# Performance work log

Hardware: AMD Instinct MI355X
Metric: run time of the kernel (lower is better)

The kernel has to match this reference:

```python
import jax, jax.numpy as jnp
import numpy as np

LN_EPS = 1e-5
N_HEADS = 8

def _layernorm(x, g, b):
    mu = jnp.mean(x, axis=-1, keepdims=True)
    var = jnp.var(x, axis=-1, keepdims=True)
    return (x - mu) * jax.lax.rsqrt(var + LN_EPS) * g + b

def _posenc(seqlen, d_model, dtype):
    den = jnp.exp(-jnp.arange(0, d_model, 2, dtype=dtype) * (np.log(10000.0) / d_model))
    pos = jnp.arange(seqlen, dtype=dtype)[:, None]  # [S,1]
    pe = jnp.zeros((seqlen, d_model), dtype=dtype)
    pe = pe.at[:, 0::2].set(jnp.sin(pos * den))
    pe = pe.at[:, 1::2].set(jnp.cos(pos * den)[:, : d_model // 2])
    return pe  # [S,d]

def setup_inputs() -> dict:
    key = jax.random.key(0)
    ks = jax.random.split(key, 12)
    B, S, V, D, F, L, DL = 64, 256, 16, 512, 2048, 6, 256
    s = 0.05
    return {
        "src_pad": jax.random.normal(ks[0], (B, S, V), jnp.float32),
        "emb_w": jax.random.normal(ks[1], (D, V), jnp.float32) * s,
        "emb_b": jnp.zeros((D,), jnp.float32),
        "qkv_w": jax.random.normal(ks[2], (L, 3 * D, D), jnp.float32) * s,
        "qkv_b": jnp.zeros((L, 3 * D), jnp.float32),
        "out_w": jax.random.normal(ks[3], (L, D, D), jnp.float32) * s,
        "out_b": jnp.zeros((L, D), jnp.float32),
        "ff1_w": jax.random.normal(ks[4], (L, F, D), jnp.float32) * s,
        "ff1_b": jnp.zeros((L, F), jnp.float32),
        "ff2_w": jax.random.normal(ks[5], (L, D, F), jnp.float32) * s,
        "ff2_b": jnp.zeros((L, D), jnp.float32),
        "ln1_g": jnp.ones((L, D), jnp.float32),
        "ln1_b": jnp.zeros((L, D), jnp.float32),
        "ln2_g": jnp.ones((L, D), jnp.float32),
        "ln2_b": jnp.zeros((L, D), jnp.float32),
        "lat_w": jax.random.normal(ks[6], (DL, S * D), jnp.float32) * 0.005,
        "lat_b": jnp.zeros((DL,), jnp.float32),
        "head_w": jax.random.normal(ks[7], (1, DL), jnp.float32) * s,
        "head_b": jnp.zeros((1,), jnp.float32),
    }

def reference(src_pad, emb_w, emb_b, qkv_w, qkv_b, out_w, out_b,
              ff1_w, ff1_b, ff2_w, ff2_b, ln1_g, ln1_b, ln2_g, ln2_b,
              lat_w, lat_b, head_w, head_b):
    B, S, V = src_pad.shape
    D = emb_w.shape[0]
    L = qkv_w.shape[0]
    H = N_HEADS
    dh = D // H
    # batched replacement of the per-token Python-loop embedding
    x = jnp.einsum('bsv,dv->bsd', src_pad, emb_w) + emb_b
    x = x + _posenc(S, D, x.dtype)  # dropout is identity at eval
    scale = 1.0 / np.sqrt(dh)
    for l in range(L):  # post-norm PyTorch TransformerEncoderLayer, relu FFN
        qkv = jnp.einsum('bsd,ed->bse', x, qkv_w[l]) + qkv_b[l]  # [B,S,3D]
        q, k, v = jnp.split(qkv, 3, axis=-1)
        q = q.reshape(B, S, H, dh).transpose(0, 2, 1, 3)
        k = k.reshape(B, S, H, dh).transpose(0, 2, 1, 3)
        v = v.reshape(B, S, H, dh).transpose(0, 2, 1, 3)
        attn = jax.nn.softmax(jnp.einsum('bhqd,bhkd->bhqk', q, k) * scale, axis=-1)
        o = jnp.einsum('bhqk,bhkd->bhqd', attn, v).transpose(0, 2, 1, 3).reshape(B, S, D)
        o = jnp.einsum('bsd,ed->bse', o, out_w[l]) + out_b[l]
        x = _layernorm(x + o, ln1_g[l], ln1_b[l])
        h = jax.nn.relu(jnp.einsum('bsd,fd->bsf', x, ff1_w[l]) + ff1_b[l])
        h = jnp.einsum('bsf,df->bsd', h, ff2_w[l]) + ff2_b[l]
        x = _layernorm(x + h, ln2_g[l], ln2_b[l])
    mem = x.reshape(B, S * D) @ lat_w.T + lat_b  # [B, d_latent]
    pred = jax.nn.sigmoid(mem @ head_w.T + head_b)  # [B,1]
    return pred
```

## Files before the change

### kernel.cpp

```cpp
#include <hip/hip_runtime.h>
#include <hip/hip_bf16.h>
#include <cstdint>

#define DEV static __device__ __forceinline__

typedef __attribute__((ext_vector_type(8))) short bf16x8;
typedef __attribute__((ext_vector_type(4))) float f32x4;

DEV unsigned short f2bf(float f) {
  union { float f; unsigned u; } c; c.f = f;
  unsigned u = c.u;
  return (unsigned short)((u + 0x7fffu + ((u >> 16) & 1u)) >> 16);
}
DEV float bf2f(unsigned short h) {
  union { unsigned u; float f; } c; c.u = ((unsigned)h) << 16; return c.f;
}
DEV unsigned pack_bf16(float a, float b) {
  union { float f; unsigned u; } ca, cb; ca.f = a; cb.f = b;
  return __builtin_amdgcn_perm(cb.u + 0x8000u, ca.u + 0x8000u, 0x07060302u);
}

#define ASYNC_COPY16(gsrc, ldst)                                                      \
  __builtin_amdgcn_global_load_lds(                                                   \
      (const __attribute__((address_space(1))) void*)(unsigned long long)(gsrc),      \
      (__attribute__((address_space(3))) void*)(unsigned int)(unsigned long long)(ldst), \
      16, 0, 0)

__global__ void cvt4_kernel(const float* __restrict__ s, unsigned short* __restrict__ d) {
  size_t i = ((size_t)blockIdx.x * 256 + threadIdx.x) * 4;
  float4 v = *(const float4*)(s + i);
  d[i + 0] = f2bf(v.x);
  d[i + 1] = f2bf(v.y);
  d[i + 2] = f2bf(v.z);
  d[i + 3] = f2bf(v.w);
}

__global__ void embed_kernel(const float* __restrict__ src,
                             const float* __restrict__ emb_w,
                             const float* __restrict__ emb_b,
                             float* __restrict__ x,
                             unsigned short* __restrict__ xb) {
  const int bs = blockIdx.x;
  const int d = threadIdx.x;
  const int s = bs & 255;
  __shared__ float sv[16];
  if (d < 16) sv[d] = src[(size_t)bs * 16 + d];
  __syncthreads();
  const float* wr = emb_w + (size_t)d * 16;
  float acc = emb_b[d];
#pragma unroll
  for (int v = 0; v < 16; v++) acc += sv[v] * wr[v];
  const float den = __expf(-(float)(d & ~1) * (9.2103403719761836f / 512.f));
  const float arg = (float)s * den;
  acc += (d & 1) ? __cosf(arg) : __sinf(arg);
  x[(size_t)bs * 512 + d] = acc;
  xb[(size_t)bs * 512 + d] = f2bf(acc);
}

template <int BN, int MINW, int RELU, int OUT_BF16, int ADD_RES>
__global__ __launch_bounds__(256, MINW) void gemm_nt(
    const unsigned short* __restrict__ A,
    const unsigned short* __restrict__ B,
    const float* __restrict__ bias,
    const float* __restrict__ res,
    float* __restrict__ Cf,
    unsigned short* __restrict__ Cb,
    int M, int N, int K) {
  constexpr int MT = (BN == 128) ? 4 : 2;
  constexpr int NT = 4;
  __shared__ unsigned short As[128 * 64];
  __shared__ unsigned short Bs[BN * 64];
  const int tid = threadIdx.x;
  const int lane = tid & 63;
  const int w = tid >> 6;
  const int m0 = blockIdx.x * 128;
  const int n0 = blockIdx.y * BN;

  const int srow = lane >> 3;
  const int scol = (((lane & 7) ^ srow)) * 8;
  const unsigned short* gA0 = A + (size_t)(m0 + w * 32 + srow) * K + scol;
  unsigned short* lA0 = As + (w * 32) * 64;
  constexpr int BROWS = BN / 4 / 8;
  const unsigned short* gB0 = B + (size_t)(n0 + w * (BN / 4) + srow) * K + scol;
  unsigned short* lB0 = Bs + (w * (BN / 4)) * 64;

  const int wm = (BN == 128) ? (w >> 1) * 64 : w * 32;
  const int wn = (BN == 128) ? (w & 1) * 64 : 0;
  const int r16 = lane & 15;
  const int quad = lane >> 4;
  const int rsw = r16 & 7;

  f32x4 acc[MT][NT] = {};

  for (int k0 = 0; k0 < K; k0 += 64) {
#pragma unroll
    for (int i = 0; i < 4; i++)
      ASYNC_COPY16(gA0 + (size_t)(i * 8) * K + k0, lA0 + i * 512);
#pragma unroll
    for (int i = 0; i < BROWS; i++)
      ASYNC_COPY16(gB0 + (size_t)(i * 8) * K + k0, lB0 + i * 512);
    __syncthreads();
#pragma unroll
    for (int kh = 0; kh < 2; kh++) {
      const int ko = ((kh * 4 + quad) ^ rsw) * 8;
      bf16x8 xa[MT], wb[NT];
#pragma unroll
      for (int i = 0; i < MT; i++)
        xa[i] = *(const bf16x8*)(As + (wm + i * 16 + r16) * 64 + ko);
#pragma unroll
      for (int j = 0; j < NT; j++)
        wb[j] = *(const bf16x8*)(Bs + (wn + j * 16 + r16) * 64 + ko);
#pragma unroll
      for (int i = 0; i < MT; i++)
#pragma unroll
        for (int j = 0; j < NT; j++)
          acc[i][j] = __builtin_amdgcn_mfma_f32_16x16x32_bf16(wb[j], xa[i], acc[i][j], 0, 0, 0);
    }
    __syncthreads();
  }

  const int mb = m0 + wm + r16;
  const int nb = n0 + wn + quad * 4;
#pragma unroll
  for (int j = 0; j < NT; j++) {
    const int n = nb + j * 16;
    const float4 bv = *(const float4*)(bias + n);
#pragma unroll
    for (int i = 0; i < MT; i++) {
      const size_t off = (size_t)(mb + i * 16) * N + n;
      float4 v;
      v.x = acc[i][j][0] + bv.x;
      v.y = acc[i][j][1] + bv.y;
      v.z = acc[i][j][2] + bv.z;
      v.w = acc[i][j][3] + bv.w;
      if (ADD_RES) {
        const float4 rr = *(const float4*)(res + off);
        v.x += rr.x; v.y += rr.y; v.z += rr.z; v.w += rr.w;
      }
      if (RELU) {
        v.x = fmaxf(v.x, 0.f); v.y = fmaxf(v.y, 0.f);
        v.z = fmaxf(v.z, 0.f); v.w = fmaxf(v.w, 0.f);
      }
      if (OUT_BF16) {
        uint2 u;
        u.x = pack_bf16(v.x, v.y);
        u.y = pack_bf16(v.z, v.w);
        *(uint2*)(Cb + off) = u;
      } else {
        *(float4*)(Cf + off) = v;
      }
    }
  }
}

__global__ __launch_bounds__(256, 2) void attn_fused(
    const unsigned short* __restrict__ qkv,
    unsigned short* __restrict__ O) {
  __shared__ unsigned short Vt[64 * 264];
  __shared__ unsigned short Pl[32 * 264];
  __shared__ float redM[4][32];
  __shared__ float redS[4][32];
  const int tid = threadIdx.x;
  const int lane = tid & 63;
  const int w = tid >> 6;
  const int r16 = lane & 15;
  const int quad = lane >> 4;
  const int h = blockIdx.x & 7;
  const int b = blockIdx.x >> 3;

  {
    const int kp = w * 32 + (lane & 31);
    const int dhalf = lane >> 5;
    const unsigned short* vbase =
        qkv + (size_t)(b * 256 + 2 * kp) * 1536 + 1024 + h * 64;
    unsigned* dst = (unsigned*)Vt;
#pragma unroll
    for (int t = 0; t < 4; t++) {
      const int dc = dhalf + 2 * t;
      const uint4 a = *(const uint4*)(vbase + dc * 8);
      const uint4 bb = *(const uint4*)(vbase + 1536 + dc * 8);
      const unsigned* ap = (const unsigned*)&a;
      const unsigned* bp = (const unsigned*)&bb;
#pragma unroll
      for (int i = 0; i < 4; i++) {
        const unsigned lo = ap[i], hi = bp[i];
        dst[(dc * 8 + 2 * i) * 132 + kp] = (lo & 0xffffu) | (hi << 16);
        dst[(dc * 8 + 2 * i + 1) * 132 + kp] = (lo >> 16) | (hi & 0xffff0000u);
      }
    }
  }
  __syncthreads();

  const unsigned short* krow =
      qkv + (size_t)(b * 256 + r16) * 1536 + 512 + h * 64 + quad * 8;
  const unsigned short* qrow =
      qkv + (size_t)(b * 256 + r16) * 1536 + h * 64 + quad * 8;

  for (int qt = 0; qt < 8; qt++) {
    const int q0 = qt * 32;
    f32x4 acc[4][2] = {};
    bf16x8 bQ0[2], bQ1[2];
#pragma unroll
    for (int nt = 0; nt < 2; nt++) {
      const unsigned short* qp = qrow + (size_t)(q0 + nt * 16) * 1536;
      bQ0[nt] = *(const bf16x8*)(qp);
      bQ1[nt] = *(const bf16x8*)(qp + 32);
    }
#pragma unroll
    for (int mt = 0; mt < 4; mt++) {
      const unsigned short* kp = krow + (size_t)(w * 64 + mt * 16) * 1536;
      const bf16x8 aK0 = *(const bf16x8*)(kp);
      const bf16x8 aK1 = *(const bf16x8*)(kp + 32);
#pragma unroll
      for (int nt = 0; nt < 2; nt++) {
        acc[mt][nt] = __builtin_amdgcn_mfma_f32_16x16x32_bf16(aK0, bQ0[nt], acc[mt][nt], 0, 0, 0);
        acc[mt][nt] = __builtin_amdgcn_mfma_f32_16x16x32_bf16(aK1, bQ1[nt], acc[mt][nt], 0, 0, 0);
      }
    }
#pragma unroll
    for (int nt = 0; nt < 2; nt++) {
      float m = acc[0][nt][0];
#pragma unroll
      for (int mt = 0; mt < 4; mt++)
#pragma unroll
        for (int r = 0; r < 4; r++) m = fmaxf(m, acc[mt][nt][r]);
      m = fmaxf(m, __shfl_xor(m, 16));
      m = fmaxf(m, __shfl_xor(m, 32));
      if (quad == 0) redM[w][nt * 16 + r16] = m;
    }
    __syncthreads();
    float mg[2], sw[2];
#pragma unroll
    for (int nt = 0; nt < 2; nt++) {
      const int q = nt * 16 + r16;
      mg[nt] = fmaxf(fmaxf(redM[0][q], redM[1][q]), fmaxf(redM[2][q], redM[3][q]));
      sw[nt] = 0.f;
    }
#pragma unroll
    for (int mt = 0; mt < 4; mt++)
#pragma unroll
      for (int nt = 0; nt < 2; nt++)
#pragma unroll
        for (int r = 0; r < 4; r++) {
          acc[mt][nt][r] = __expf((acc[mt][nt][r] - mg[nt]) * 0.125f);
          sw[nt] += acc[mt][nt][r];
        }
#pragma unroll
    for (int nt = 0; nt < 2; nt++) {
      sw[nt] += __shfl_xor(sw[nt], 16);
      sw[nt] += __shfl_xor(sw[nt], 32);
      if (quad == 0) redS[w][nt * 16 + r16] = sw[nt];
    }
    __syncthreads();
    float inv[2];
#pragma unroll
    for (int nt = 0; nt < 2; nt++) {
      const int q = nt * 16 + r16;
      inv[nt] = 1.f / (redS[0][q] + redS[1][q] + redS[2][q] + redS[3][q]);
    }
#pragma unroll
    for (int nt = 0; nt < 2; nt++) {
      unsigned short* prow = Pl + (nt * 16 + r16) * 264 + w * 64 + quad * 4;
#pragma unroll
      for (int mt = 0; mt < 4; mt++) {
        uint2 u;
        u.x = pack_bf16(acc[mt][nt][0] * inv[nt], acc[mt][nt][1] * inv[nt]);
        u.y = pack_bf16(acc[mt][nt][2] * inv[nt], acc[mt][nt][3] * inv[nt]);
        *(uint2*)(prow + mt * 16) = u;
      }
    }
    __syncthreads();
    f32x4 o[2] = {};
#pragma unroll
    for (int s = 0; s < 8; s++) {
      const bf16x8 aV = *(const bf16x8*)(Vt + (w * 16 + r16) * 264 + s * 32 + quad * 8);
#pragma unroll
      for (int nt = 0; nt < 2; nt++) {
        const bf16x8 bP = *(const bf16x8*)(Pl + (nt * 16 + r16) * 264 + s * 32 + quad * 8);
        o[nt] = __builtin_amdgcn_mfma_f32_16x16x32_bf16(aV, bP, o[nt], 0, 0, 0);
      }
    }
#pragma unroll
    for (int nt = 0; nt < 2; nt++) {
      uint2 u;
      u.x = pack_bf16(o[nt][0], o[nt][1]);
      u.y = pack_bf16(o[nt][2], o[nt][3]);
      *(uint2*)(O + (size_t)(b * 256 + q0 + nt * 16 + r16) * 512 + h * 64 +
                w * 16 + quad * 4) = u;
    }
  }
}

__global__ __launch_bounds__(256) void ln_kernel(
    const float* __restrict__ z, const float* __restrict__ g,
    const float* __restrict__ bb, float* __restrict__ x,
    unsigned short* __restrict__ xb) {
  const int row = blockIdx.x;
  const int tid = threadIdx.x;
  const size_t base = (size_t)row * 512;
  float v0 = z[base + tid];
  float v1 = z[base + tid + 256];
  float s = v0 + v1, ss = v0 * v0 + v1 * v1;
#pragma unroll
  for (int off = 32; off > 0; off >>= 1) {
    s += __shfl_xor(s, off);
    ss += __shfl_xor(ss, off);
  }
  __shared__ float red[8];
  const int w = tid >> 6, lane = tid & 63;
  if (lane == 0) { red[w * 2] = s; red[w * 2 + 1] = ss; }
  __syncthreads();
  s = red[0] + red[2] + red[4] + red[6];
  ss = red[1] + red[3] + red[5] + red[7];
  const float mu = s * (1.f / 512.f);
  const float var = ss * (1.f / 512.f) - mu * mu;
  const float rs = rsqrtf(var + 1e-5f);
  const float o0 = (v0 - mu) * rs * g[tid] + bb[tid];
  const float o1 = (v1 - mu) * rs * g[tid + 256] + bb[tid + 256];
  x[base + tid] = o0;
  x[base + tid + 256] = o1;
  xb[base + tid] = f2bf(o0);
  xb[base + tid + 256] = f2bf(o1);
}

__global__ void zero_kernel(float* __restrict__ p) {
  p[blockIdx.x * 256 + threadIdx.x] = 0.f;
}

__global__ __launch_bounds__(256) void latent_gemm(
    const unsigned short* __restrict__ xb, const float* __restrict__ W,
    float* __restrict__ mem) {
  const int tid = threadIdx.x;
  const int lane = tid & 63;
  const int w = tid >> 6;
  const int r16 = lane & 15;
  const int quad = lane >> 4;
  const int n0 = blockIdx.x * 64 + w * 16;
  const int kc0 = blockIdx.y * 1024;

  const float* wrow = W + (size_t)(n0 + r16) * 131072 + kc0 + quad * 8;
  const unsigned short* xrow = xb + (size_t)r16 * 131072 + kc0 + quad * 8;

  f32x4 c[4] = {};
  for (int k = 0; k < 1024; k += 32) {
    const float4 wa = *(const float4*)(wrow + k);
    const float4 wb = *(const float4*)(wrow + k + 4);
    union { unsigned u[4]; bf16x8 v; } cw;
    cw.u[0] = pack_bf16(wa.x, wa.y);
    cw.u[1] = pack_bf16(wa.z, wa.w);
    cw.u[2] = pack_bf16(wb.x, wb.y);
    cw.u[3] = pack_bf16(wb.z, wb.w);
#pragma unroll
    for (int i = 0; i < 4; i++) {
      const bf16x8 aX = *(const bf16x8*)(xrow + (size_t)i * 2097152 + k);
      c[i] = __builtin_amdgcn_mfma_f32_16x16x32_bf16(aX, cw.v, c[i], 0, 0, 0);
    }
  }
#pragma unroll
  for (int i = 0; i < 4; i++)
#pragma unroll
    for (int r = 0; r < 4; r++)
      atomicAdd(&mem[(size_t)(i * 16 + quad * 4 + r) * 256 + n0 + r16], c[i][r]);
}

__global__ __launch_bounds__(256) void head_kernel(
    const float* __restrict__ mem, const float* __restrict__ lat_b,
    const float* __restrict__ head_w, const float* __restrict__ head_b,
    float* __restrict__ out) {
  const int b = blockIdx.x;
  const int tid = threadIdx.x;
  float v = (mem[(size_t)b * 256 + tid] + lat_b[tid]) * head_w[tid];
#pragma unroll
  for (int off = 32; off > 0; off >>= 1) v += __shfl_xor(v, off);
  __shared__ float red[4];
  const int w = tid >> 6, lane = tid & 63;
  if (lane == 0) red[w] = v;
  __syncthreads();
  if (tid == 0) {
    const float z = red[0] + red[1] + red[2] + red[3] + head_b[0];
    out[b] = 1.f / (1.f + __expf(-z));
  }
}

extern "C" void kernel_launch(void* const* d_in, const int* in_sizes, int n_in,
                              void* d_out, int out_size, void* d_ws, size_t ws_size,
                              hipStream_t stream) {
  (void)in_sizes; (void)n_in; (void)out_size; (void)ws_size;
  const float* src_pad = (const float*)d_in[0];
  const float* emb_w = (const float*)d_in[1];
  const float* emb_b = (const float*)d_in[2];
  const float* qkv_w = (const float*)d_in[3];
  const float* qkv_b = (const float*)d_in[4];
  const float* out_w = (const float*)d_in[5];
  const float* out_b = (const float*)d_in[6];
  const float* ff1_w = (const float*)d_in[7];
  const float* ff1_b = (const float*)d_in[8];
  const float* ff2_w = (const float*)d_in[9];
  const float* ff2_b = (const float*)d_in[10];
  const float* ln1_g = (const float*)d_in[11];
  const float* ln1_b = (const float*)d_in[12];
  const float* ln2_g = (const float*)d_in[13];
  const float* ln2_b = (const float*)d_in[14];
  const float* lat_w = (const float*)d_in[15];
  const float* lat_b = (const float*)d_in[16];
  const float* head_w = (const float*)d_in[17];
  const float* head_b = (const float*)d_in[18];
  float* out = (float*)d_out;

  char* p = (char*)d_ws;
  float* x = (float*)p;             p += (size_t)16384 * 512 * 4;
  unsigned short* xb = (unsigned short*)p; p += (size_t)16384 * 512 * 2;
  unsigned short* qkv = (unsigned short*)p;
  float* y = (float*)qkv;
  p += (size_t)16384 * 1536 * 2;
  unsigned short* attno = (unsigned short*)p; p += (size_t)16384 * 512 * 2;
  unsigned short* h = (unsigned short*)p;     p += (size_t)16384 * 2048 * 2;
  unsigned short* wq = (unsigned short*)p;    p += (size_t)4718592 * 2;
  unsigned short* wo = (unsigned short*)p;    p += (size_t)1572864 * 2;
  unsigned short* wf1 = (unsigned short*)p;   p += (size_t)6291456 * 2;
  unsigned short* wf2 = (unsigned short*)p;   p += (size_t)6291456 * 2;
  float* mem = (float*)p;           p += (size_t)16384 * 4;

  cvt4_kernel<<<4608, 256, 0, stream>>>(qkv_w, wq);
  cvt4_kernel<<<1536, 256, 0, stream>>>(out_w, wo);
  cvt4_kernel<<<6144, 256, 0, stream>>>(ff1_w, wf1);
  cvt4_kernel<<<6144, 256, 0, stream>>>(ff2_w, wf2);

  embed_kernel<<<16384, 512, 0, stream>>>(src_pad, emb_w, emb_b, x, xb);

  for (int l = 0; l < 6; l++) {
    gemm_nt<128, 3, 0, 1, 0><<<dim3(128, 12), 256, 0, stream>>>(
        xb, wq + (size_t)l * 786432, qkv_b + (size_t)l * 1536, nullptr,
        nullptr, qkv, 16384, 1536, 512);
    attn_fused<<<512, 256, 0, stream>>>(qkv, attno);
    gemm_nt<64, 4, 0, 0, 1><<<dim3(128, 8), 256, 0, stream>>>(
        attno, wo + (size_t)l * 262144, out_b + (size_t)l * 512, x,
        y, nullptr, 16384, 512, 512);
    ln_kernel<<<16384, 256, 0, stream>>>(y, ln1_g + (size_t)l * 512,
                                         ln1_b + (size_t)l * 512, x, xb);
    gemm_nt<128, 3, 1, 1, 0><<<dim3(128, 16), 256, 0, stream>>>(
        xb, wf1 + (size_t)l * 1048576, ff1_b + (size_t)l * 2048, nullptr,
        nullptr, h, 16384, 2048, 512);
    gemm_nt<64, 4, 0, 0, 1><<<dim3(128, 8), 256, 0, stream>>>(
        h, wf2 + (size_t)l * 1048576, ff2_b + (size_t)l * 512, x,
        y, nullptr, 16384, 512, 2048);
    ln_kernel<<<16384, 256, 0, stream>>>(y, ln2_g + (size_t)l * 512,
                                         ln2_b + (size_t)l * 512, x, xb);
  }

  zero_kernel<<<64, 256, 0, stream>>>(mem);
  latent_gemm<<<dim3(4, 128), 256, 0, stream>>>(xb, lat_w, mem);
  head_kernel<<<64, 256, 0, stream>>>(mem, lat_b, head_w, head_b, out);
}
```

Baseline: 1.726 ms.

## Fuse out-proj and FF2 GEMMs with residual add and LayerNorm

After: 1.897 ms. 1.1x slower.

```diff
diff --git a/kernel.cpp b/kernel.cpp
--- a/kernel.cpp
+++ b/kernel.cpp
@@ -57,63 +57,57 @@
   xb[(size_t)bs * 512 + d] = f2bf(acc);
 }
 
-template <int BN, int MINW, int RELU, int OUT_BF16, int ADD_RES>
-__global__ __launch_bounds__(256, MINW) void gemm_nt(
+template <int RELU>
+__global__ __launch_bounds__(256, 3) void gemm_nt(
     const unsigned short* __restrict__ A,
     const unsigned short* __restrict__ B,
     const float* __restrict__ bias,
-    const float* __restrict__ res,
-    float* __restrict__ Cf,
     unsigned short* __restrict__ Cb,
     int M, int N, int K) {
-  constexpr int MT = (BN == 128) ? 4 : 2;
-  constexpr int NT = 4;
   __shared__ unsigned short As[128 * 64];
-  __shared__ unsigned short Bs[BN * 64];
+  __shared__ unsigned short Bs[128 * 64];
   const int tid = threadIdx.x;
   const int lane = tid & 63;
   const int w = tid >> 6;
   const int m0 = blockIdx.x * 128;
-  const int n0 = blockIdx.y * BN;
+  const int n0 = blockIdx.y * 128;
 
   const int srow = lane >> 3;
   const int scol = (((lane & 7) ^ srow)) * 8;
   const unsigned short* gA0 = A + (size_t)(m0 + w * 32 + srow) * K + scol;
   unsigned short* lA0 = As + (w * 32) * 64;
-  constexpr int BROWS = BN / 4 / 8;
-  const unsigned short* gB0 = B + (size_t)(n0 + w * (BN / 4) + srow) * K + scol;
-  unsigned short* lB0 = Bs + (w * (BN / 4)) * 64;
-
-  const int wm = (BN == 128) ? (w >> 1) * 64 : w * 32;
-  const int wn = (BN == 128) ? (w & 1) * 64 : 0;
+  const unsigned short* gB0 = B + (size_t)(n0 + w * 32 + srow) * K + scol;
+  unsigned short* lB0 = Bs + (w * 32) * 64;
+
+  const int wm = (w >> 1) * 64;
+  const int wn = (w & 1) * 64;
   const int r16 = lane & 15;
   const int quad = lane >> 4;
   const int rsw = r16 & 7;
 
-  f32x4 acc[MT][NT] = {};
+  f32x4 acc[4][4] = {};
 
   for (int k0 = 0; k0 < K; k0 += 64) {
 #pragma unroll
-    for (int i = 0; i < 4; i++)
+    for (int i = 0; i < 4; i++) {
       ASYNC_COPY16(gA0 + (size_t)(i * 8) * K + k0, lA0 + i * 512);
-#pragma unroll
-    for (int i = 0; i < BROWS; i++)
       ASYNC_COPY16(gB0 + (size_t)(i * 8) * K + k0, lB0 + i * 512);
+    }
     __syncthreads();
 #pragma unroll
     for (int kh = 0; kh < 2; kh++) {
       const int ko = ((kh * 4 + quad) ^ rsw) * 8;
-      bf16x8 xa[MT], wb[NT];
-#pragma unroll
-      for (int i = 0; i < MT; i++)
+      bf16x8 xa[4], wb[4];
+#pragma unroll
+      for (int i = 0; i < 4; i++)
         xa[i] = *(const bf16x8*)(As + (wm + i * 16 + r16) * 64 + ko);
 #pragma unroll
-      for (int j = 0; j < NT; j++)
+      for (int j = 0; j < 4; j++)
         wb[j] = *(const bf16x8*)(Bs + (wn + j * 16 + r16) * 64 + ko);
 #pragma unroll
-      for (int i = 0; i < MT; i++)
-#pragma unroll
-        for (int j = 0; j < NT; j++)
+      for (int i = 0; i < 4; i++)
+#pragma unroll
+        for (int j = 0; j < 4; j++)
           acc[i][j] = __builtin_amdgcn_mfma_f32_16x16x32_bf16(wb[j], xa[i], acc[i][j], 0, 0, 0);
     }
     __syncthreads();
@@ -122,33 +116,125 @@
   const int mb = m0 + wm + r16;
   const int nb = n0 + wn + quad * 4;
 #pragma unroll
-  for (int j = 0; j < NT; j++) {
+  for (int j = 0; j < 4; j++) {
     const int n = nb + j * 16;
     const float4 bv = *(const float4*)(bias + n);
 #pragma unroll
-    for (int i = 0; i < MT; i++) {
+    for (int i = 0; i < 4; i++) {
       const size_t off = (size_t)(mb + i * 16) * N + n;
       float4 v;
       v.x = acc[i][j][0] + bv.x;
       v.y = acc[i][j][1] + bv.y;
       v.z = acc[i][j][2] + bv.z;
       v.w = acc[i][j][3] + bv.w;
-      if (ADD_RES) {
-        const float4 rr = *(const float4*)(res + off);
-        v.x += rr.x; v.y += rr.y; v.z += rr.z; v.w += rr.w;
-      }
       if (RELU) {
         v.x = fmaxf(v.x, 0.f); v.y = fmaxf(v.y, 0.f);
         v.z = fmaxf(v.z, 0.f); v.w = fmaxf(v.w, 0.f);
       }
-      if (OUT_BF16) {
-        uint2 u;
-        u.x = pack_bf16(v.x, v.y);
-        u.y = pack_bf16(v.z, v.w);
-        *(uint2*)(Cb + off) = u;
-      } else {
-        *(float4*)(Cf + off) = v;
-      }
+      uint2 u;
+      u.x = pack_bf16(v.x, v.y);
+      u.y = pack_bf16(v.z, v.w);
+      *(uint2*)(Cb + off) = u;
+    }
+  }
+}
+
+__global__ __launch_bounds__(256, 2) void gemm_ln(
+    const unsigned short* __restrict__ A,
+    const unsigned short* __restrict__ B,
+    const float* __restrict__ bias,
+    const float* __restrict__ g,
+    const float* __restrict__ bb,
+    float* __restrict__ x,
+    unsigned short* __restrict__ xb,
+    int K) {
+  __shared__ unsigned short As[32 * 32];
+  __shared__ unsigned short Bs[512 * 32];
+  __shared__ float redS[4][2][16];
+  __shared__ float redQ[4][2][16];
+  const int tid = threadIdx.x;
+  const int lane = tid & 63;
+  const int w = tid >> 6;
+  const int r16 = lane & 15;
+  const int quad = lane >> 4;
+  const int m0 = blockIdx.x * 32;
+
+  const int srow = lane >> 2;
+  const int scol = ((lane & 3) ^ ((srow >> 1) & 3)) * 8;
+  const unsigned short* gB0 = B + (size_t)(w * 128 + srow) * K + scol;
+  unsigned short* lB0 = Bs + (w * 128) * 32;
+  const unsigned short* gA0 = A + (size_t)(m0 + (w & 1) * 16 + srow) * K + scol;
+  unsigned short* lA0 = As + ((w & 1) * 16) * 32;
+
+  const int ko = (quad ^ ((r16 >> 1) & 3)) * 8;
+
+  f32x4 acc[2][8] = {};
+
+  for (int k0 = 0; k0 < K; k0 += 32) {
+    if (w < 2) ASYNC_COPY16(gA0 + k0, lA0);
+#pragma unroll
+    for (int i = 0; i < 8; i++)
+      ASYNC_COPY16(gB0 + (size_t)(i * 16) * K + k0, lB0 + i * 512);
+    __syncthreads();
+    bf16x8 xa[2], wv[8];
+#pragma unroll
+    for (int i = 0; i < 2; i++)
+      xa[i] = *(const bf16x8*)(As + (i * 16 + r16) * 32 + ko);
+#pragma unroll
+    for (int j = 0; j < 8; j++)
+      wv[j] = *(const bf16x8*)(Bs + (w * 128 + j * 16 + r16) * 32 + ko);
+#pragma unroll
+    for (int i = 0; i < 2; i++)
+#pragma unroll
+      for (int j = 0; j < 8; j++)
+        acc[i][j] = __builtin_amdgcn_mfma_f32_16x16x32_bf16(wv[j], xa[i], acc[i][j], 0, 0, 0);
+    __syncthreads();
+  }
+
+#pragma unroll
+  for (int i = 0; i < 2; i++) {
+    const int m = m0 + i * 16 + r16;
+    float s = 0.f, q = 0.f;
+#pragma unroll
+    for (int j = 0; j < 8; j++) {
+      const int n = w * 128 + j * 16 + quad * 4;
+      const float4 bv = *(const float4*)(bias + n);
+      const float4 rr = *(const float4*)(x + (size_t)m * 512 + n);
+      acc[i][j][0] += bv.x + rr.x;
+      acc[i][j][1] += bv.y + rr.y;
+      acc[i][j][2] += bv.z + rr.z;
+      acc[i][j][3] += bv.w + rr.w;
+      s += acc[i][j][0] + acc[i][j][1] + acc[i][j][2] + acc[i][j][3];
+      q += acc[i][j][0] * acc[i][j][0] + acc[i][j][1] * acc[i][j][1] +
+           acc[i][j][2] * acc[i][j][2] + acc[i][j][3] * acc[i][j][3];
+    }
+    s += __shfl_xor(s, 16); s += __shfl_xor(s, 32);
+    q += __shfl_xor(q, 16); q += __shfl_xor(q, 32);
+    if (quad == 0) { redS[w][i][r16] = s; redQ[w][i][r16] = q; }
+  }
+  __syncthreads();
+#pragma unroll
+  for (int i = 0; i < 2; i++) {
+    const int m = m0 + i * 16 + r16;
+    const float st = redS[0][i][r16] + redS[1][i][r16] + redS[2][i][r16] + redS[3][i][r16];
+    const float qt = redQ[0][i][r16] + redQ[1][i][r16] + redQ[2][i][r16] + redQ[3][i][r16];
+    const float mu = st * (1.f / 512.f);
+    const float rs = rsqrtf(qt * (1.f / 512.f) - mu * mu + 1e-5f);
+#pragma unroll
+    for (int j = 0; j < 8; j++) {
+      const int n = w * 128 + j * 16 + quad * 4;
+      const float4 gv = *(const float4*)(g + n);
+      const float4 b2 = *(const float4*)(bb + n);
+      float4 v;
+      v.x = (acc[i][j][0] - mu) * rs * gv.x + b2.x;
+      v.y = (acc[i][j][1] - mu) * rs * gv.y + b2.y;
+      v.z = (acc[i][j][2] - mu) * rs * gv.z + b2.z;
+      v.w = (acc[i][j][3] - mu) * rs * gv.w + b2.w;
+      *(float4*)(x + (size_t)m * 512 + n) = v;
+      uint2 u;
+      u.x = pack_bf16(v.x, v.y);
+      u.y = pack_bf16(v.z, v.w);
+      *(uint2*)(xb + (size_t)m * 512 + n) = u;
     }
   }
 }
@@ -289,38 +375,6 @@
                 w * 16 + quad * 4) = u;
     }
   }
-}
-
-__global__ __launch_bounds__(256) void ln_kernel(
-    const float* __restrict__ z, const float* __restrict__ g,
-    const float* __restrict__ bb, float* __restrict__ x,
-    unsigned short* __restrict__ xb) {
-  const int row = blockIdx.x;
-  const int tid = threadIdx.x;
-  const size_t base = (size_t)row * 512;
-  float v0 = z[base + tid];
-  float v1 = z[base + tid + 256];
-  float s = v0 + v1, ss = v0 * v0 + v1 * v1;
-#pragma unroll
-  for (int off = 32; off > 0; off >>= 1) {
-    s += __shfl_xor(s, off);
-    ss += __shfl_xor(ss, off);
-  }
-  __shared__ float red[8];
-  const int w = tid >> 6, lane = tid & 63;
-  if (lane == 0) { red[w * 2] = s; red[w * 2 + 1] = ss; }
-  __syncthreads();
-  s = red[0] + red[2] + red[4] + red[6];
-  ss = red[1] + red[3] + red[5] + red[7];
-  const float mu = s * (1.f / 512.f);
-  const float var = ss * (1.f / 512.f) - mu * mu;
-  const float rs = rsqrtf(var + 1e-5f);
-  const float o0 = (v0 - mu) * rs * g[tid] + bb[tid];
-  const float o1 = (v1 - mu) * rs * g[tid + 256] + bb[tid + 256];
-  x[base + tid] = o0;
-  x[base + tid + 256] = o1;
-  xb[base + tid] = f2bf(o0);
-  xb[base + tid + 256] = f2bf(o1);
 }
 
 __global__ void zero_kernel(float* __restrict__ p) {
@@ -410,9 +464,7 @@
   char* p = (char*)d_ws;
   float* x = (float*)p;             p += (size_t)16384 * 512 * 4;
   unsigned short* xb = (unsigned short*)p; p += (size_t)16384 * 512 * 2;
-  unsigned short* qkv = (unsigned short*)p;
-  float* y = (float*)qkv;
-  p += (size_t)16384 * 1536 * 2;
+  unsigned short* qkv = (unsigned short*)p; p += (size_t)16384 * 1536 * 2;
   unsigned short* attno = (unsigned short*)p; p += (size_t)16384 * 512 * 2;
   unsigned short* h = (unsigned short*)p;     p += (size_t)16384 * 2048 * 2;
   unsigned short* wq = (unsigned short*)p;    p += (size_t)4718592 * 2;
@@ -429,23 +481,19 @@
   embed_kernel<<<16384, 512, 0, stream>>>(src_pad, emb_w, emb_b, x, xb);
 
   for (int l = 0; l < 6; l++) {
-    gemm_nt<128, 3, 0, 1, 0><<<dim3(128, 12), 256, 0, stream>>>(
-        xb, wq + (size_t)l * 786432, qkv_b + (size_t)l * 1536, nullptr,
-        nullptr, qkv, 16384, 1536, 512);
+    gemm_nt<0><<<dim3(128, 12), 256, 0, stream>>>(
+        xb, wq + (size_t)l * 786432, qkv_b + (size_t)l * 1536,
+        qkv, 16384, 1536, 512);
     attn_fused<<<512, 256, 0, stream>>>(qkv, attno);
-    gemm_nt<64, 4, 0, 0, 1><<<dim3(128, 8), 256, 0, stream>>>(
-        attno, wo + (size_t)l * 262144, out_b + (size_t)l * 512, x,
-        y, nullptr, 16384, 512, 512);
-    ln_kernel<<<16384, 256, 0, stream>>>(y, ln1_g + (size_t)l * 512,
-                                         ln1_b + (size_t)l * 512, x, xb);
-    gemm_nt<128, 3, 1, 1, 0><<<dim3(128, 16), 256, 0, stream>>>(
-        xb, wf1 + (size_t)l * 1048576, ff1_b + (size_t)l * 2048, nullptr,
-        nullptr, h, 16384, 2048, 512);
-    gemm_nt<64, 4, 0, 0, 1><<<dim3(128, 8), 256, 0, stream>>>(
-        h, wf2 + (size_t)l * 1048576, ff2_b + (size_t)l * 512, x,
-        y, nullptr, 16384, 512, 2048);
-    ln_kernel<<<16384, 256, 0, stream>>>(y, ln2_g + (size_t)l * 512,
-                                         ln2_b + (size_t)l * 512, x, xb);
+    gemm_ln<<<512, 256, 0, stream>>>(
+        attno, wo + (size_t)l * 262144, out_b + (size_t)l * 512,
+        ln1_g + (size_t)l * 512, ln1_b + (size_t)l * 512, x, xb, 512);
+    gemm_nt<1><<<dim3(128, 16), 256, 0, stream>>>(
+        xb, wf1 + (size_t)l * 1048576, ff1_b + (size_t)l * 2048,
+        h, 16384, 2048, 512);
+    gemm_ln<<<512, 256, 0, stream>>>(
+        h, wf2 + (size_t)l * 1048576, ff2_b + (size_t)l * 512,
+        ln2_g + (size_t)l * 512, ln2_b + (size_t)l * 512, x, xb, 2048);
   }
 
   zero_kernel<<<64, 256, 0, stream>>>(mem);
```
